# Performance work log

Measured on AMD Instinct MI355X. Metric: run time of the kernel, lower is better.

Reference implementation:

```python
import jax, jax.numpy as jnp
import numpy as np

B, T, HID = 8, 2048, 1024
NH, MD = 16, 16
UFC = 2  # len(use_for_context) = ['lr', 'rl']
MAT_EPS = 1e-5
VEC_EPS = 1e-6
SQRT_MD = float(np.sqrt(MD))


def setup_inputs() -> dict:
    key = jax.random.key(0)
    ks = jax.random.split(key, 5)
    s_in = 1.0 / np.sqrt(HID)
    s_out = 1.0 / np.sqrt(NH * MD * UFC)
    return {
        "hidden_states": jax.random.normal(ks[0], (B, T, HID), jnp.float32),
        "W_mat": jax.random.uniform(ks[1], (HID, NH * MD * MD), jnp.float32, -s_in, s_in),
        "b_mat": jax.random.uniform(ks[2], (NH * MD * MD,), jnp.float32, -s_in, s_in),
        "W_out": jax.random.uniform(ks[3], (NH * MD * UFC, HID), jnp.float32, -s_out, s_out),
        "b_out": jax.random.uniform(ks[4], (HID,), jnp.float32, -s_out, s_out),
    }


def _scan_vectors(m, v0, reverse):
    """Sequential matrix-vector recurrence with per-step L2 normalization.
    m: (T, B*NH, d, d); v0: (B*NH, d). Returns history (T, B*NH, d)
    (equal to torch history[1:] for lr, and reversed(history[1:]) for rl)."""
    def step(v, m_t):
        nv = jnp.einsum('bij,bj->bi', m_t, v)
        nv = nv / (jnp.linalg.norm(nv, axis=-1, keepdims=True) + VEC_EPS)
        return nv, nv
    _, hist = jax.lax.scan(step, v0, m, reverse=reverse)
    return hist


def reference(hidden_states, W_mat, b_mat, W_out, b_out):
    # predict_matrix: fc_to_mat + Frobenius matrix normalization ([-2,-1] branch)
    m = hidden_states @ W_mat + b_mat                       # (B, T, NH*MD*MD)
    m = m.reshape(B, T, NH, MD, MD).transpose(1, 0, 2, 3, 4)  # (T, B, NH, d, d)
    fro = jnp.linalg.norm(m, axis=(-2, -1), keepdims=True)
    m_norm = m / (fro + MAT_EPS) * SQRT_MD
    m_norm = m_norm.reshape(T, B * NH, MD, MD)

    # init_type == 'one': v[..., 0, :] = 1 -> e_0
    v0 = jnp.zeros((B * NH, MD), jnp.float32).at[:, 0].set(1.0)

    v_lr = _scan_vectors(m_norm, v0, reverse=False)  # (T, B*NH, d)
    v_rl = _scan_vectors(m_norm, v0, reverse=True)   # (T, B*NH, d)

    def to_bthd(v):
        return v.reshape(T, B, NH, MD).transpose(1, 0, 2, 3)  # (B, T, NH, d)

    x = jnp.concatenate([to_bthd(v_lr), to_bthd(v_rl)], axis=-1)  # (B, T, NH, 2d)
    # networks_for_heads == 'common': flatten heads, Linear, gelu (exact erf form)
    x = x.reshape(B, T, NH * MD * UFC) @ W_out + b_out
    return jax.nn.gelu(x, approximate=False)
```

## Files before the change

kernel.cpp:

```cpp
#include <hip/hip_runtime.h>
#include <math.h>

#define Tdim 2048
#define HIDd 1024
#define NHd 16
#define NCOL 4096
#define Cn 64
#define Ln 32
#define LSTR 40
#define KCAT 3072
#define KB 6144

typedef _Float16 f16x4  __attribute__((ext_vector_type(4)));
typedef _Float16 f16x8  __attribute__((ext_vector_type(8)));
typedef float    f32x4  __attribute__((ext_vector_type(4)));

typedef __attribute__((address_space(1))) void gvoid_t;
typedef __attribute__((address_space(3))) void lvoid_t;

__global__ __launch_bounds__(256) void conv_A_kernel(const float* __restrict__ hs,
                                                     _Float16* __restrict__ Ac)
{
    const size_t i = ((size_t)blockIdx.x * 256 + threadIdx.x) * 8;
    const size_t r = i >> 10, k = i & 1023;
    const float4 x0 = *(const float4*)(hs + i);
    const float4 x1 = *(const float4*)(hs + i + 4);
    const float v[8] = {x0.x, x0.y, x0.z, x0.w, x1.x, x1.y, x1.z, x1.w};
    f16x8 h, hm, l;
#pragma unroll
    for (int j = 0; j < 8; ++j) {
        const _Float16 hh = (_Float16)v[j];
        h[j]  = hh;
        hm[j] = (_Float16)(v[j] * 0.03125f);
        l[j]  = (_Float16)((v[j] - (float)hh) * 32.0f);
    }
    _Float16* o = Ac + r * KCAT + k;
    *(f16x8*)(o)        = h;
    *(f16x8*)(o + 1024) = hm;
    *(f16x8*)(o + 2048) = l;
}

__global__ __launch_bounds__(256) void conv_B_kernel(const float* __restrict__ W,
                                                     _Float16* __restrict__ Bc)
{
    __shared__ float t[32][33];
    const int tx = threadIdx.x & 31, ty = threadIdx.x >> 5;
    const int n0 = blockIdx.x * 32, k0 = blockIdx.y * 32;
#pragma unroll
    for (int i = 0; i < 4; ++i)
        t[ty + i * 8][tx] = W[(size_t)(k0 + ty + i * 8) * NCOL + n0 + tx];
    __syncthreads();
#pragma unroll
    for (int i = 0; i < 4; ++i) {
        const float w = t[tx][ty + i * 8];
        const _Float16 h = (_Float16)w;
        const size_t o = (size_t)(n0 + ty + i * 8) * KCAT + k0 + tx;
        Bc[o]        = h;
        Bc[o + 1024] = (_Float16)((w - (float)h) * 32.0f);
        Bc[o + 2048] = (_Float16)((float)h * 0.03125f);
    }
}

__global__ __launch_bounds__(256) void conv_W2T_kernel(const float* __restrict__ W,
                                                       _Float16* __restrict__ WT)
{
    __shared__ float t[32][33];
    const int tx = threadIdx.x & 31, ty = threadIdx.x >> 5;
    const int n0 = blockIdx.x * 32, k0 = blockIdx.y * 32;
#pragma unroll
    for (int i = 0; i < 4; ++i)
        t[ty + i * 8][tx] = W[(size_t)(k0 + ty + i * 8) * 1024 + n0 + tx];
    __syncthreads();
#pragma unroll
    for (int i = 0; i < 4; ++i)
        WT[(size_t)(n0 + ty + i * 8) * 512 + k0 + tx] = (_Float16)t[tx][ty + i * 8];
}

#define MFMA_PHASE(CPH) \
    _Pragma("unroll") \
    for (int m2_ = 0; m2_ < 2; ++m2_) { \
        _Pragma("unroll") \
        for (int nt_ = 0; nt_ < 4; ++nt_) { \
            acc[(CPH)*2 + m2_][nt_] = __builtin_amdgcn_mfma_f32_16x16x32_f16(af[m2_][0], bf[nt_][0], acc[(CPH)*2 + m2_][nt_], 0, 0, 0); \
            acc[(CPH)*2 + m2_][nt_] = __builtin_amdgcn_mfma_f32_16x16x32_f16(af[m2_][1], bf[nt_][1], acc[(CPH)*2 + m2_][nt_], 0, 0, 0); \
        } \
    }

#define PHASE(BUF, CPH, STAGE_EXPR, DOGATE) do { \
    af[0][0] = readA(BUF, (CPH)*2,     0); \
    af[0][1] = readA(BUF, (CPH)*2,     1); \
    af[1][0] = readA(BUF, (CPH)*2 + 1, 0); \
    af[1][1] = readA(BUF, (CPH)*2 + 1, 1); \
    if ((CPH) == 0) { \
        _Pragma("unroll") \
        for (int nt_ = 0; nt_ < 4; ++nt_) { bf[nt_][0] = readB(BUF, nt_, 0); bf[nt_][1] = readB(BUF, nt_, 1); } \
    } \
    STAGE_EXPR; \
    asm volatile("s_barrier" ::: "memory"); \
    asm volatile("s_waitcnt lgkmcnt(0)" ::: "memory"); \
    __builtin_amdgcn_sched_barrier(0); \
    __builtin_amdgcn_s_setprio(1); \
    MFMA_PHASE(CPH) \
    __builtin_amdgcn_s_setprio(0); \
    if (DOGATE) { \
        if (notlast) asm volatile("s_waitcnt vmcnt(6)" ::: "memory"); \
        else         asm volatile("s_waitcnt vmcnt(0)" ::: "memory"); \
    } \
    asm volatile("s_barrier" ::: "memory"); \
} while (0)

__global__ __launch_bounds__(512, 2) void gemm1_8ph(const _Float16* __restrict__ A,
                                                    const _Float16* __restrict__ B,
                                                    const float* __restrict__ bias,
                                                    float* __restrict__ Mout)
{
    __shared__ __align__(16) _Float16 sA[2][256 * 64];
    __shared__ __align__(16) _Float16 sB[2][256 * 64];
    const int tid = threadIdx.x;
    const int lane = tid & 63;
    const int wid = tid >> 6;
    const int wm = wid >> 2, wn = wid & 3;
    const int q = lane >> 4, ln = lane & 15;
    const int col0 = blockIdx.x * 256;
    const int row0 = blockIdx.y * 256;

    const char* Ab = (const char*)A + (size_t)row0 * KB;
    const char* Bb = (const char*)B + (size_t)col0 * KB;

    auto stage_chunk = [&](const char* g, int fr, int kt, char* ldsbase) {
        const int rr = tid >> 3;
        const int cb = (tid & 7) << 4;
        const char* src = g + (size_t)(fr + rr) * KB + (size_t)kt * 128 + (cb ^ ((rr & 7) << 4));
        char* dst = ldsbase + ((tid >> 6) << 10);
        __builtin_amdgcn_global_load_lds((gvoid_t*)src, (lvoid_t*)dst, 16, 0, 0);
    };
    auto stageA2 = [&](int b, int t, int h) {
        stage_chunk(Ab, h * 64,       t, (char*)&sA[b][0] + (size_t)(h * 64) * 128);
        stage_chunk(Ab, 128 + h * 64, t, (char*)&sA[b][0] + (size_t)(128 + h * 64) * 128);
    };
    auto stageB2 = [&](int b, int t, int h) {
        stage_chunk(Bb, h * 128,      t, (char*)&sB[b][0] + (size_t)(h * 128) * 128);
        stage_chunk(Bb, h * 128 + 64, t, (char*)&sB[b][0] + (size_t)(h * 128 + 64) * 128);
    };
    auto readA = [&](int b, int mf, int ks) -> f16x8 {
        const int r = wm * 128 + mf * 16 + ln;
        return *(const f16x8*)((const char*)&sA[b][0] + r * 128 + ((ks * 64 + q * 16) ^ ((r & 7) << 4)));
    };
    auto readB = [&](int b, int nt, int ks) -> f16x8 {
        const int r = wn * 64 + nt * 16 + ln;
        return *(const f16x8*)((const char*)&sB[b][0] + r * 128 + ((ks * 64 + q * 16) ^ ((r & 7) << 4)));
    };

    stageB2(0, 0, 0); stageB2(0, 0, 1); stageA2(0, 0, 0); stageA2(0, 0, 1);
    stageB2(1, 1, 0); stageB2(1, 1, 1); stageA2(1, 1, 0);

    f32x4 acc[8][4];
    const f32x4 z4 = {0.f, 0.f, 0.f, 0.f};
#pragma unroll
    for (int mf = 0; mf < 8; ++mf)
#pragma unroll
        for (int nt = 0; nt < 4; ++nt) acc[mf][nt] = z4;

    asm volatile("s_waitcnt vmcnt(6)" ::: "memory");
    asm volatile("s_barrier" ::: "memory");

    f16x8 af[2][2];
    f16x8 bf[4][2];

#pragma unroll 1
    for (int it = 0; it < 24; ++it) {
        const int t0 = it * 2;
        const bool notlast = (it != 23);
        PHASE(0, 0, (stageA2(1, t0 + 1, 1)), 0);
        PHASE(0, 1, (notlast ? stageB2(0, t0 + 2, 0) : (void)0), 0);
        PHASE(0, 2, (notlast ? stageB2(0, t0 + 2, 1) : (void)0), 0);
        PHASE(0, 3, (notlast ? stageA2(0, t0 + 2, 0) : (void)0), 1);
        PHASE(1, 0, (notlast ? stageA2(0, t0 + 2, 1) : (void)0), 0);
        PHASE(1, 1, (notlast ? stageB2(1, t0 + 3, 0) : (void)0), 0);
        PHASE(1, 2, (notlast ? stageB2(1, t0 + 3, 1) : (void)0), 0);
        PHASE(1, 3, (notlast ? stageA2(1, t0 + 3, 0) : (void)0), 1);
    }

#pragma unroll
    for (int nt = 0; nt < 4; ++nt) {
        const int c = col0 + wn * 64 + nt * 16 + ln;
        const float bv = bias[c];
        const int h = c >> 8, e = c & 255;
#pragma unroll
        for (int mf = 0; mf < 8; ++mf) {
#pragma unroll
            for (int r = 0; r < 4; ++r) {
                const int row = row0 + wm * 128 + mf * 16 + q * 4 + r;
                const int bbl = row >> 11, t = row & 2047;
                Mout[((size_t)(bbl * 16 + h) * Tdim + t) * 256 + e] = acc[mf][nt][r] + bv;
            }
        }
    }
}

__global__ __launch_bounds__(256) void stageA_mfma(const float* __restrict__ m,
                                                   float* __restrict__ q, int SS)
{
    const int tid = threadIdx.x;
    const int wave = tid >> 6, lane = tid & 63;
    const int qd = lane >> 4, ln = lane & 15;
    const int chain = blockIdx.x * 4 + wave;
    const int seq = chain >> 6, c = chain & (Cn - 1);
    const float* mp = m + ((size_t)seq * Tdim + c * Ln) * 256;

    float vlr[4], vrl[4];
#pragma unroll
    for (int r = 0; r < 4; ++r) {
        const float iv = (qd * 4 + r == ln) ? 1.0f : 0.0f;
        vlr[r] = iv; vrl[r] = iv;
    }

    float4 arow = *(const float4*)(mp + ln * 16 + qd * 4);
    float acol[4];
#pragma unroll
    for (int i = 0; i < 4; ++i) acol[i] = mp[(4 * qd + i) * 16 + ln];
    float f2 = arow.x*arow.x + arow.y*arow.y + arow.z*arow.z + arow.w*arow.w;
#pragma unroll
    for (int off = 1; off < 64; off <<= 1) f2 += __shfl_xor(f2, off);
    float sm = 4.0f * rsqrtf(f2 + 1e-12f);

    for (int s = 0; s < Ln; ++s) {
        f16x4 mhr, mlr2, mhc, mlc;
        const float ar[4] = {arow.x * sm, arow.y * sm, arow.z * sm, arow.w * sm};
#pragma unroll
        for (int i = 0; i < 4; ++i) {
            _Float16 h = (_Float16)ar[i];
            mhr[i] = h; mlr2[i] = (_Float16)((ar[i] - (float)h) * 1024.0f);
            const float v = acol[i] * sm;
            h = (_Float16)v;
            mhc[i] = h; mlc[i] = (_Float16)((v - (float)h) * 1024.0f);
        }
        float smn = sm;
        if (s + 1 < Ln) {
            const float* Mn = mp + (s + 1) * 256;
            arow = *(const float4*)(Mn + ln * 16 + qd * 4);
#pragma unroll
            for (int i = 0; i < 4; ++i) acol[i] = Mn[(4 * qd + i) * 16 + ln];
            float f2n = arow.x*arow.x + arow.y*arow.y + arow.z*arow.z + arow.w*arow.w;
#pragma unroll
            for (int off = 1; off < 64; off <<= 1) f2n += __shfl_xor(f2n, off);
            smn = 4.0f * rsqrtf(f2n + 1e-12f);
        }
        f16x4 qh1, ql1, qh2, ql2;
#pragma unroll
        for (int r = 0; r < 4; ++r) {
            _Float16 h = (_Float16)vlr[r];
            qh1[r] = h; ql1[r] = (_Float16)((vlr[r] - (float)h) * 1024.0f);
            h = (_Float16)vrl[r];
            qh2[r] = h; ql2[r] = (_Float16)((vrl[r] - (float)h) * 1024.0f);
        }
        f32x4 a1 = {0.f,0.f,0.f,0.f}, a2 = {0.f,0.f,0.f,0.f};
        f32x4 b1 = {0.f,0.f,0.f,0.f}, b2 = {0.f,0.f,0.f,0.f};
        a1 = __builtin_amdgcn_mfma_f32_16x16x16f16(mhr,  qh1, a1, 0, 0, 0);
        a2 = __builtin_amdgcn_mfma_f32_16x16x16f16(mhr,  ql1, a2, 0, 0, 0);
        a2 = __builtin_amdgcn_mfma_f32_16x16x16f16(mlr2, qh1, a2, 0, 0, 0);
        b1 = __builtin_amdgcn_mfma_f32_16x16x16f16(mhc,  qh2, b1, 0, 0, 0);
        b2 = __builtin_amdgcn_mfma_f32_16x16x16f16(mhc,  ql2, b2, 0, 0, 0);
        b2 = __builtin_amdgcn_mfma_f32_16x16x16f16(mlc,  qh2, b2, 0, 0, 0);

        float mx1 = 0.f, mx2 = 0.f;
#pragma unroll
        for (int r = 0; r < 4; ++r) {
            vlr[r] = a1[r] + a2[r] * (1.0f / 1024.0f);
            vrl[r] = b1[r] + b2[r] * (1.0f / 1024.0f);
            mx1 = fmaxf(mx1, fabsf(vlr[r]));
            mx2 = fmaxf(mx2, fabsf(vrl[r]));
        }
#pragma unroll
        for (int off = 1; off < 64; off <<= 1) {
            mx1 = fmaxf(mx1, __shfl_xor(mx1, off));
            mx2 = fmaxf(mx2, __shfl_xor(mx2, off));
        }
        const float i1 = 1.0f / (mx1 + 1e-30f);
        const float i2 = 1.0f / (mx2 + 1e-30f);
#pragma unroll
        for (int r = 0; r < 4; ++r) { vlr[r] *= i1; vrl[r] *= i2; }
        sm = smn;
    }

    float ss = 0.f, st = 0.f;
#pragma unroll
    for (int r = 0; r < 4; ++r) { ss += vlr[r]*vlr[r]; st += vrl[r]*vrl[r]; }
#pragma unroll
    for (int off = 1; off < 64; off <<= 1) { ss += __shfl_xor(ss, off); st += __shfl_xor(st, off); }
    const float sl = 1.0f / (sqrtf(ss) + 1e-30f);
    const float sr = 1.0f / (sqrtf(st) + 1e-30f);
    float* qlr_out = q + ((size_t)seq * Cn + c) * 256;
    float* qrl_out = q + ((size_t)(SS + seq) * Cn + c) * 256;
#pragma unroll
    for (int r = 0; r < 4; ++r)
        qlr_out[(qd * 4 + r) * 16 + ln] = vlr[r] * sl;
    float4 qv; qv.x = vrl[0]*sr; qv.y = vrl[1]*sr; qv.z = vrl[2]*sr; qv.w = vrl[3]*sr;
    *(float4*)(qrl_out + ln * 16 + qd * 4) = qv;
}

__global__ __launch_bounds__(64) void stageB_kernel(const float* __restrict__ q,
                                                    float* __restrict__ vs, int SS)
{
    const int lane = threadIdx.x & 63;
    const int i = lane & 15;
    const int chain = blockIdx.x;
    const int dir = (chain >= SS) ? 1 : 0;
    const int seq = chain - dir * SS;
    const float* qb = q + (size_t)(dir * SS + seq) * Cn * 256;
    float* vb = vs + (size_t)(dir * SS + seq) * Cn * 16;

    float myw = (i == 0) ? 1.0f : 0.0f;
    float wv[16];
#pragma unroll
    for (int k2 = 0; k2 < 16; ++k2) wv[k2] = (k2 == 0) ? 1.0f : 0.0f;

    int cc = dir ? (Cn - 1) : 0;
    const float* Qp = qb + (size_t)cc * 256 + i * 16;
    float4 q0 = *(const float4*)(Qp + 0);
    float4 q1 = *(const float4*)(Qp + 4);
    float4 q2 = *(const float4*)(Qp + 8);
    float4 q3 = *(const float4*)(Qp + 12);

    for (int s = 0; s < Cn; ++s) {
        vb[cc * 16 + i] = myw;
        float nv = q0.x*wv[0] + q0.y*wv[1] + q0.z*wv[2] + q0.w*wv[3]
                 + q1.x*wv[4] + q1.y*wv[5] + q1.z*wv[6] + q1.w*wv[7]
                 + q2.x*wv[8] + q2.y*wv[9] + q2.z*wv[10] + q2.w*wv[11]
                 + q3.x*wv[12] + q3.y*wv[13] + q3.z*wv[14] + q3.w*wv[15];
        if (s + 1 < Cn) {
            const int ccn = dir ? (Cn - 2 - s) : (s + 1);
            const float* Qn = qb + (size_t)ccn * 256 + i * 16;
            q0 = *(const float4*)(Qn + 0);
            q1 = *(const float4*)(Qn + 4);
            q2 = *(const float4*)(Qn + 8);
            q3 = *(const float4*)(Qn + 12);
        }
        float s2 = nv * nv;
        s2 += __shfl_xor(s2, 1); s2 += __shfl_xor(s2, 2);
        s2 += __shfl_xor(s2, 4); s2 += __shfl_xor(s2, 8);
        const float wn = nv / (sqrtf(s2) + 1e-20f);
        myw = wn;
#pragma unroll
        for (int k2 = 0; k2 < 16; ++k2) wv[k2] = __shfl(wn, (lane & 48) | k2);
        cc = dir ? (Cn - 2 - s) : (s + 1);
    }
}

__global__ __launch_bounds__(256) void stageC_kernel(const float* __restrict__ m,
                                                     const float* __restrict__ vs,
                                                     _Float16* __restrict__ x, int SS)
{
    __shared__ float vbuf[16][16];
    const int tid = threadIdx.x;
    const int lane = tid & 63;
    const int j = lane & 15;
    const int grp = tid >> 4;
    const int chain = blockIdx.x * 16 + grp;
    const int dir = chain & 1;
    const int sc = chain >> 1;
    const int c = sc & (Cn - 1), seq = sc >> 6;
    const int bbl = seq >> 4, h = seq & 15;

    vbuf[grp][j] = vs[((size_t)(dir * SS + seq) * Cn + c) * 16 + j];

    const int t0 = c * Ln;
    int t = dir ? (t0 + Ln - 1) : t0;
    const float* Mp = m + ((size_t)seq * Tdim + t) * 256 + j * 16;
    float4 r0 = *(const float4*)(Mp + 0);
    float4 r1 = *(const float4*)(Mp + 4);
    float4 r2 = *(const float4*)(Mp + 8);
    float4 r3 = *(const float4*)(Mp + 12);

    for (int s = 0; s < Ln; ++s) {
        const int tcur = t;
        const float4 w0 = *(const float4*)&vbuf[grp][0];
        const float4 w1 = *(const float4*)&vbuf[grp][4];
        const float4 w2 = *(const float4*)&vbuf[grp][8];
        const float4 w3 = *(const float4*)&vbuf[grp][12];
        float nv = r0.x*w0.x + r0.y*w0.y + r0.z*w0.z + r0.w*w0.w
                 + r1.x*w1.x + r1.y*w1.y + r1.z*w1.z + r1.w*w1.w
                 + r2.x*w2.x + r2.y*w2.y + r2.z*w2.z + r2.w*w2.w
                 + r3.x*w3.x + r3.y*w3.y + r3.z*w3.z + r3.w*w3.w;
        if (s + 1 < Ln) {
            t = dir ? (t0 + Ln - 2 - s) : (t0 + s + 1);
            const float* Mn = m + ((size_t)seq * Tdim + t) * 256 + j * 16;
            r0 = *(const float4*)(Mn + 0);
            r1 = *(const float4*)(Mn + 4);
            r2 = *(const float4*)(Mn + 8);
            r3 = *(const float4*)(Mn + 12);
        }
        float s2 = nv * nv;
        s2 += __shfl_xor(s2, 1); s2 += __shfl_xor(s2, 2);
        s2 += __shfl_xor(s2, 4); s2 += __shfl_xor(s2, 8);
        const float vn = nv / (sqrtf(s2) + 1e-6f);
        x[(((size_t)bbl * Tdim + tcur) * NHd + h) * 32 + dir * 16 + j] = (_Float16)vn;
        vbuf[grp][j] = vn;
    }
}

__global__ __launch_bounds__(256) void gemm2_f16(const _Float16* __restrict__ A,
                                                 const _Float16* __restrict__ BT,
                                                 const float* __restrict__ bias,
                                                 float* __restrict__ out, int row0)
{
    __shared__ _Float16 Al[128 * LSTR];
    __shared__ _Float16 Bl[128 * LSTR];
    const int tid = threadIdx.x;
    const int wave = tid >> 6, lane = tid & 63;
    const int wm = wave & 1, wn = wave >> 1;
    const int qd = lane >> 4, ln = lane & 15;
    const int r0 = blockIdx.y * 128;
    const int c0 = blockIdx.x * 128;

    f32x4 acc[4][4] = {{{0.f,0.f,0.f,0.f}}};

    const int sr = tid >> 2, sc = tid & 3;
    const _Float16* Ag = A  + (size_t)(r0 + sr) * 512 + sc * 8;
    const _Float16* Bg = BT + (size_t)(c0 + sr) * 512 + sc * 8;
    _Float16* Alw = &Al[sr * LSTR + sc * 8];
    _Float16* Blw = &Bl[sr * LSTR + sc * 8];

    for (int k0 = 0; k0 < 512; k0 += 32) {
        const f16x8 a0 = *(const f16x8*)(Ag + k0);
        const f16x8 a1 = *(const f16x8*)(Ag + (size_t)64 * 512 + k0);
        const f16x8 b0 = *(const f16x8*)(Bg + k0);
        const f16x8 b1 = *(const f16x8*)(Bg + (size_t)64 * 512 + k0);
        __syncthreads();
        *(f16x8*)(Alw)             = a0;
        *(f16x8*)(Alw + 64 * LSTR) = a1;
        *(f16x8*)(Blw)             = b0;
        *(f16x8*)(Blw + 64 * LSTR) = b1;
        __syncthreads();
        f16x8 af[4], bfr[4];
#pragma unroll
        for (int mt = 0; mt < 4; ++mt)
            af[mt] = *(const f16x8*)&Al[(wm * 64 + mt * 16 + ln) * LSTR + qd * 8];
#pragma unroll
        for (int nt = 0; nt < 4; ++nt)
            bfr[nt] = *(const f16x8*)&Bl[(wn * 64 + nt * 16 + ln) * LSTR + qd * 8];
#pragma unroll
        for (int mt = 0; mt < 4; ++mt)
#pragma unroll
            for (int nt = 0; nt < 4; ++nt)
                acc[mt][nt] = __builtin_amdgcn_mfma_f32_16x16x32_f16(af[mt], bfr[nt], acc[mt][nt], 0, 0, 0);
    }
#pragma unroll
    for (int nt = 0; nt < 4; ++nt) {
        const int c = c0 + wn * 64 + nt * 16 + ln;
        const float bv = bias[c];
#pragma unroll
        for (int mt = 0; mt < 4; ++mt) {
#pragma unroll
            for (int r = 0; r < 4; ++r) {
                const int row = r0 + wm * 64 + mt * 16 + qd * 4 + r;
                float v = acc[mt][nt][r] + bv;
                v = 0.5f * v * (1.0f + erff(v * 0.70710678118654752f));
                out[(size_t)(row0 + row) * 1024 + c] = v;
            }
        }
    }
}

extern "C" void kernel_launch(void* const* d_in, const int* in_sizes, int n_in,
                              void* d_out, int out_size, void* d_ws, size_t ws_size,
                              hipStream_t stream)
{
    const float* hs    = (const float*)d_in[0];
    const float* W_mat = (const float*)d_in[1];
    const float* b_mat = (const float*)d_in[2];
    const float* W_out = (const float*)d_in[3];
    const float* b_out = (const float*)d_in[4];
    float* out = (float*)d_out;

    const size_t per_bb = (32ull << 20) + (2ull << 20) + (12ull << 20) + (128ull << 10);
    const size_t wbase  = 25ull << 20;
    int nbb = 8;
    while (nbb > 1 && ws_size < wbase + (size_t)nbb * per_bb) nbb >>= 1;

    char* base = (char*)d_ws;
    _Float16* W2T = (_Float16*)base;
    _Float16* Bc  = (_Float16*)(base + (1ull << 20));
    size_t off = wbase;
    float* m  = (float*)(base + off);  off += (size_t)nbb * (32ull << 20);
    float* qx = (float*)(base + off);  off += (size_t)nbb * (2ull << 20);
    _Float16* Ac = (_Float16*)(base + off); off += (size_t)nbb * (12ull << 20);
    float* vs = (float*)(base + off);

    conv_B_kernel<<<dim3(128, 32), 256, 0, stream>>>(W_mat, Bc);
    conv_W2T_kernel<<<dim3(32, 16), 256, 0, stream>>>(W_out, W2T);

    for (int bb0 = 0; bb0 < 8; bb0 += nbb) {
        const int row0 = bb0 * Tdim;
        const int SS = nbb * 16;
        conv_A_kernel<<<nbb * 1024, 256, 0, stream>>>(hs + (size_t)row0 * HIDd, Ac);
        gemm1_8ph<<<dim3(16, nbb * 8), 512, 0, stream>>>(Ac, Bc, b_mat, m);
        stageA_mfma<<<nbb * 256, 256, 0, stream>>>(m, qx, SS);
        stageB_kernel<<<nbb * 32, 64, 0, stream>>>(qx, vs, SS);
        stageC_kernel<<<nbb * 128, 256, 0, stream>>>(m, vs, (_Float16*)qx, SS);
        gemm2_f16<<<dim3(8, nbb * 16), 256, 0, stream>>>((_Float16*)qx, W2T, b_out, out, row0);
    }
}
```

Measured before the change: 854.2 us.

## Store per-step chunk prefix products so stage C skips the sequential scan

Stage A now keeps each chunk's intermediate prefix matrix products (one per step, scaled by max only every other step) as fp16 in a new workspace buffer P. It runs one wave per direction in 128-thread blocks. Stage C then rebuilds each timestep's vector as an independent dot product of the stored prefix with the chunk's entry vector, followed by normalisation, so the serial per-step recurrence over m is removed and steps run in parallel. The cost is an extra 32 MB per batch slice of fp16 writes and reads, plus the accuracy risk of fp16 prefixes and of skipping rescaling on alternate steps. The larger workspace can also force a smaller batch grouping.

```diff
diff --git a/kernel.cpp b/kernel.cpp
--- a/kernel.cpp
+++ b/kernel.cpp
@@ -198,105 +198,89 @@
     }
 }
 
-__global__ __launch_bounds__(256) void stageA_mfma(const float* __restrict__ m,
-                                                   float* __restrict__ q, int SS)
+__global__ __launch_bounds__(128) void stageA2_mfma(const float* __restrict__ m,
+                                                    float* __restrict__ q,
+                                                    _Float16* __restrict__ P, int SS)
 {
     const int tid = threadIdx.x;
-    const int wave = tid >> 6, lane = tid & 63;
+    const int dir = tid >> 6;
+    const int lane = tid & 63;
     const int qd = lane >> 4, ln = lane & 15;
-    const int chain = blockIdx.x * 4 + wave;
-    const int seq = chain >> 6, c = chain & (Cn - 1);
+    const int sc = blockIdx.x;
+    const int seq = sc >> 6, c = sc & (Cn - 1);
     const float* mp = m + ((size_t)seq * Tdim + c * Ln) * 256;
-
-    float vlr[4], vrl[4];
-#pragma unroll
-    for (int r = 0; r < 4; ++r) {
-        const float iv = (qd * 4 + r == ln) ? 1.0f : 0.0f;
-        vlr[r] = iv; vrl[r] = iv;
-    }
-
-    float4 arow = *(const float4*)(mp + ln * 16 + qd * 4);
-    float acol[4];
-#pragma unroll
-    for (int i = 0; i < 4; ++i) acol[i] = mp[(4 * qd + i) * 16 + ln];
+    _Float16* Pp = P + (((size_t)(dir * SS + seq) * Cn + c) * Ln) * 256
+                     + (qd * 4) * 16 + ln;
+
+    float v[4];
+#pragma unroll
+    for (int r = 0; r < 4; ++r) v[r] = (qd * 4 + r == ln) ? 1.0f : 0.0f;
+
+    const int dstep = dir ? -256 : 256;
+    const float* Ms = mp + (dir ? (Ln - 1) * 256 : 0) + ln * 16 + qd * 4;
+
+    float4 arow = *(const float4*)Ms;
     float f2 = arow.x*arow.x + arow.y*arow.y + arow.z*arow.z + arow.w*arow.w;
 #pragma unroll
     for (int off = 1; off < 64; off <<= 1) f2 += __shfl_xor(f2, off);
     float sm = 4.0f * rsqrtf(f2 + 1e-12f);
 
     for (int s = 0; s < Ln; ++s) {
-        f16x4 mhr, mlr2, mhc, mlc;
+        f16x4 mh, mlo;
         const float ar[4] = {arow.x * sm, arow.y * sm, arow.z * sm, arow.w * sm};
 #pragma unroll
         for (int i = 0; i < 4; ++i) {
-            _Float16 h = (_Float16)ar[i];
-            mhr[i] = h; mlr2[i] = (_Float16)((ar[i] - (float)h) * 1024.0f);
-            const float v = acol[i] * sm;
-            h = (_Float16)v;
-            mhc[i] = h; mlc[i] = (_Float16)((v - (float)h) * 1024.0f);
+            const _Float16 h = (_Float16)ar[i];
+            mh[i] = h; mlo[i] = (_Float16)((ar[i] - (float)h) * 1024.0f);
         }
         float smn = sm;
         if (s + 1 < Ln) {
-            const float* Mn = mp + (s + 1) * 256;
-            arow = *(const float4*)(Mn + ln * 16 + qd * 4);
-#pragma unroll
-            for (int i = 0; i < 4; ++i) acol[i] = Mn[(4 * qd + i) * 16 + ln];
+            Ms += dstep;
+            arow = *(const float4*)Ms;
             float f2n = arow.x*arow.x + arow.y*arow.y + arow.z*arow.z + arow.w*arow.w;
 #pragma unroll
             for (int off = 1; off < 64; off <<= 1) f2n += __shfl_xor(f2n, off);
             smn = 4.0f * rsqrtf(f2n + 1e-12f);
         }
-        f16x4 qh1, ql1, qh2, ql2;
+        f16x4 qh, ql;
 #pragma unroll
         for (int r = 0; r < 4; ++r) {
-            _Float16 h = (_Float16)vlr[r];
-            qh1[r] = h; ql1[r] = (_Float16)((vlr[r] - (float)h) * 1024.0f);
-            h = (_Float16)vrl[r];
-            qh2[r] = h; ql2[r] = (_Float16)((vrl[r] - (float)h) * 1024.0f);
+            const _Float16 h = (_Float16)v[r];
+            qh[r] = h; ql[r] = (_Float16)((v[r] - (float)h) * 1024.0f);
         }
         f32x4 a1 = {0.f,0.f,0.f,0.f}, a2 = {0.f,0.f,0.f,0.f};
-        f32x4 b1 = {0.f,0.f,0.f,0.f}, b2 = {0.f,0.f,0.f,0.f};
-        a1 = __builtin_amdgcn_mfma_f32_16x16x16f16(mhr,  qh1, a1, 0, 0, 0);
-        a2 = __builtin_amdgcn_mfma_f32_16x16x16f16(mhr,  ql1, a2, 0, 0, 0);
-        a2 = __builtin_amdgcn_mfma_f32_16x16x16f16(mlr2, qh1, a2, 0, 0, 0);
-        b1 = __builtin_amdgcn_mfma_f32_16x16x16f16(mhc,  qh2, b1, 0, 0, 0);
-        b2 = __builtin_amdgcn_mfma_f32_16x16x16f16(mhc,  ql2, b2, 0, 0, 0);
-        b2 = __builtin_amdgcn_mfma_f32_16x16x16f16(mlc,  qh2, b2, 0, 0, 0);
-
-        float mx1 = 0.f, mx2 = 0.f;
-#pragma unroll
-        for (int r = 0; r < 4; ++r) {
-            vlr[r] = a1[r] + a2[r] * (1.0f / 1024.0f);
-            vrl[r] = b1[r] + b2[r] * (1.0f / 1024.0f);
-            mx1 = fmaxf(mx1, fabsf(vlr[r]));
-            mx2 = fmaxf(mx2, fabsf(vrl[r]));
-        }
-#pragma unroll
-        for (int off = 1; off < 64; off <<= 1) {
-            mx1 = fmaxf(mx1, __shfl_xor(mx1, off));
-            mx2 = fmaxf(mx2, __shfl_xor(mx2, off));
-        }
-        const float i1 = 1.0f / (mx1 + 1e-30f);
-        const float i2 = 1.0f / (mx2 + 1e-30f);
-#pragma unroll
-        for (int r = 0; r < 4; ++r) { vlr[r] *= i1; vrl[r] *= i2; }
+        a1 = __builtin_amdgcn_mfma_f32_16x16x16f16(mh,  qh, a1, 0, 0, 0);
+        a2 = __builtin_amdgcn_mfma_f32_16x16x16f16(mh,  ql, a2, 0, 0, 0);
+        a2 = __builtin_amdgcn_mfma_f32_16x16x16f16(mlo, qh, a2, 0, 0, 0);
+#pragma unroll
+        for (int r = 0; r < 4; ++r) v[r] = a1[r] + a2[r] * (1.0f / 1024.0f);
+
+        if (s & 1) {
+            float mx = 0.f;
+#pragma unroll
+            for (int r = 0; r < 4; ++r) mx = fmaxf(mx, fabsf(v[r]));
+#pragma unroll
+            for (int off = 1; off < 64; off <<= 1) mx = fmaxf(mx, __shfl_xor(mx, off));
+            const float inv = 1.0f / (mx + 1e-30f);
+#pragma unroll
+            for (int r = 0; r < 4; ++r) v[r] *= inv;
+        }
+#pragma unroll
+        for (int r = 0; r < 4; ++r)
+            Pp[(size_t)s * 256 + r * 16] = (_Float16)v[r];
         sm = smn;
     }
 
-    float ss = 0.f, st = 0.f;
-#pragma unroll
-    for (int r = 0; r < 4; ++r) { ss += vlr[r]*vlr[r]; st += vrl[r]*vrl[r]; }
-#pragma unroll
-    for (int off = 1; off < 64; off <<= 1) { ss += __shfl_xor(ss, off); st += __shfl_xor(st, off); }
+    float ss = 0.f;
+#pragma unroll
+    for (int r = 0; r < 4; ++r) ss += v[r] * v[r];
+#pragma unroll
+    for (int off = 1; off < 64; off <<= 1) ss += __shfl_xor(ss, off);
     const float sl = 1.0f / (sqrtf(ss) + 1e-30f);
-    const float sr = 1.0f / (sqrtf(st) + 1e-30f);
-    float* qlr_out = q + ((size_t)seq * Cn + c) * 256;
-    float* qrl_out = q + ((size_t)(SS + seq) * Cn + c) * 256;
+    float* qo = q + ((size_t)(dir * SS + seq) * Cn + c) * 256;
 #pragma unroll
     for (int r = 0; r < 4; ++r)
-        qlr_out[(qd * 4 + r) * 16 + ln] = vlr[r] * sl;
-    float4 qv; qv.x = vrl[0]*sr; qv.y = vrl[1]*sr; qv.z = vrl[2]*sr; qv.w = vrl[3]*sr;
-    *(float4*)(qrl_out + ln * 16 + qd * 4) = qv;
+        qo[(qd * 4 + r) * 16 + ln] = v[r] * sl;
 }
 
 __global__ __launch_bounds__(64) void stageB_kernel(const float* __restrict__ q,
@@ -347,55 +331,43 @@
     }
 }
 
-__global__ __launch_bounds__(256) void stageC_kernel(const float* __restrict__ m,
-                                                     const float* __restrict__ vs,
-                                                     _Float16* __restrict__ x, int SS)
-{
-    __shared__ float vbuf[16][16];
+__global__ __launch_bounds__(256) void stageC2_kernel(const _Float16* __restrict__ P,
+                                                      const float* __restrict__ vs,
+                                                      _Float16* __restrict__ x, int SS)
+{
     const int tid = threadIdx.x;
-    const int lane = tid & 63;
-    const int j = lane & 15;
-    const int grp = tid >> 4;
-    const int chain = blockIdx.x * 16 + grp;
-    const int dir = chain & 1;
-    const int sc = chain >> 1;
-    const int c = sc & (Cn - 1), seq = sc >> 6;
+    const int wave = tid >> 6, lane = tid & 63;
+    const int dsc = blockIdx.x * 4 + wave;
+    const int dirseq = dsc >> 6, c = dsc & (Cn - 1);
+    const int dir = (dirseq >= SS) ? 1 : 0;
+    const int seq = dirseq - dir * SS;
     const int bbl = seq >> 4, h = seq & 15;
-
-    vbuf[grp][j] = vs[((size_t)(dir * SS + seq) * Cn + c) * 16 + j];
-
+    const _Float16* Pp = P + (size_t)dsc * (Ln * 256);
+    const float* vp = vs + (size_t)dsc * 16;
+
+    float v[16];
+#pragma unroll
+    for (int k = 0; k < 16; ++k) v[k] = vp[k];
+
+    const int tt = lane >> 4, j = lane & 15;
     const int t0 = c * Ln;
-    int t = dir ? (t0 + Ln - 1) : t0;
-    const float* Mp = m + ((size_t)seq * Tdim + t) * 256 + j * 16;
-    float4 r0 = *(const float4*)(Mp + 0);
-    float4 r1 = *(const float4*)(Mp + 4);
-    float4 r2 = *(const float4*)(Mp + 8);
-    float4 r3 = *(const float4*)(Mp + 12);
-
-    for (int s = 0; s < Ln; ++s) {
-        const int tcur = t;
-        const float4 w0 = *(const float4*)&vbuf[grp][0];
-        const float4 w1 = *(const float4*)&vbuf[grp][4];
-        const float4 w2 = *(const float4*)&vbuf[grp][8];
-        const float4 w3 = *(const float4*)&vbuf[grp][12];
-        float nv = r0.x*w0.x + r0.y*w0.y + r0.z*w0.z + r0.w*w0.w
-                 + r1.x*w1.x + r1.y*w1.y + r1.z*w1.z + r1.w*w1.w
-                 + r2.x*w2.x + r2.y*w2.y + r2.z*w2.z + r2.w*w2.w
-                 + r3.x*w3.x + r3.y*w3.y + r3.z*w3.z + r3.w*w3.w;
-        if (s + 1 < Ln) {
-            t = dir ? (t0 + Ln - 2 - s) : (t0 + s + 1);
-            const float* Mn = m + ((size_t)seq * Tdim + t) * 256 + j * 16;
-            r0 = *(const float4*)(Mn + 0);
-            r1 = *(const float4*)(Mn + 4);
-            r2 = *(const float4*)(Mn + 8);
-            r3 = *(const float4*)(Mn + 12);
-        }
+#pragma unroll
+    for (int g = 0; g < 8; ++g) {
+        const int s = g * 4 + tt;
+        const _Float16* pr = Pp + (size_t)s * 256 + j * 16;
+        const f16x8 p0 = *(const f16x8*)(pr);
+        const f16x8 p1 = *(const f16x8*)(pr + 8);
+        float nv = 0.f;
+#pragma unroll
+        for (int k = 0; k < 8; ++k) nv += (float)p0[k] * v[k];
+#pragma unroll
+        for (int k = 0; k < 8; ++k) nv += (float)p1[k] * v[k + 8];
         float s2 = nv * nv;
         s2 += __shfl_xor(s2, 1); s2 += __shfl_xor(s2, 2);
         s2 += __shfl_xor(s2, 4); s2 += __shfl_xor(s2, 8);
         const float vn = nv / (sqrtf(s2) + 1e-6f);
-        x[(((size_t)bbl * Tdim + tcur) * NHd + h) * 32 + dir * 16 + j] = (_Float16)vn;
-        vbuf[grp][j] = vn;
+        const int t = dir ? (t0 + Ln - 1 - s) : (t0 + s);
+        x[(((size_t)bbl * Tdim + t) * NHd + h) * 32 + dir * 16 + j] = (_Float16)vn;
     }
 }
 
@@ -473,7 +445,8 @@
     const float* b_out = (const float*)d_in[4];
     float* out = (float*)d_out;
 
-    const size_t per_bb = (32ull << 20) + (2ull << 20) + (12ull << 20) + (128ull << 10);
+    const size_t per_bb = (32ull << 20) + (2ull << 20) + (12ull << 20) + (32ull << 20)
+                        + (128ull << 10);
     const size_t wbase  = 25ull << 20;
     int nbb = 8;
     while (nbb > 1 && ws_size < wbase + (size_t)nbb * per_bb) nbb >>= 1;
@@ -485,6 +458,7 @@
     float* m  = (float*)(base + off);  off += (size_t)nbb * (32ull << 20);
     float* qx = (float*)(base + off);  off += (size_t)nbb * (2ull << 20);
     _Float16* Ac = (_Float16*)(base + off); off += (size_t)nbb * (12ull << 20);
+    _Float16* P  = (_Float16*)(base + off); off += (size_t)nbb * (32ull << 20);
     float* vs = (float*)(base + off);
 
     conv_B_kernel<<<dim3(128, 32), 256, 0, stream>>>(W_mat, Bc);
@@ -495,9 +469,9 @@
         const int SS = nbb * 16;
         conv_A_kernel<<<nbb * 1024, 256, 0, stream>>>(hs + (size_t)row0 * HIDd, Ac);
         gemm1_8ph<<<dim3(16, nbb * 8), 512, 0, stream>>>(Ac, Bc, b_mat, m);
-        stageA_mfma<<<nbb * 256, 256, 0, stream>>>(m, qx, SS);
-        stageB_kernel<<<nbb * 32, 64, 0, stream>>>(qx, vs, SS);
-        stageC_kernel<<<nbb * 128, 256, 0, stream>>>(m, vs, (_Float16*)qx, SS);
+        stageA2_mfma<<<SS * 64, 128, 0, stream>>>(m, qx, P, SS);
+        stageB_kernel<<<2 * SS, 64, 0, stream>>>(qx, vs, SS);
+        stageC2_kernel<<<SS * 32, 256, 0, stream>>>(P, vs, (_Float16*)qx, SS);
         gemm2_f16<<<dim3(8, nbb * 16), 256, 0, stream>>>((_Float16*)qx, W2T, b_out, out, row0);
     }
 }
```

After: 941.6 us. 1.1x slower.
